# Kernel optimization log

Measured on AMD Instinct MI355X. Metric: run time of the kernel, lower is better.

Reference implementation:

```python
import jax, jax.numpy as jnp
import numpy as np

H = 1024


def setup_inputs() -> dict:
    key = jax.random.key(0)
    ks = jax.random.split(key, 8)
    B, S = 32, 2048
    query = jax.random.normal(ks[0], (B, 1, H), dtype=jnp.float32)
    keys = jax.random.normal(ks[1], (B, S, H), dtype=jnp.float32)
    s = 1.0 / np.sqrt(H)
    Wa_w = jax.random.uniform(ks[2], (H, H), jnp.float32, -s, s)
    Wa_b = jax.random.uniform(ks[3], (H,), jnp.float32, -s, s)
    Ua_w = jax.random.uniform(ks[4], (H, H), jnp.float32, -s, s)
    Ua_b = jax.random.uniform(ks[5], (H,), jnp.float32, -s, s)
    Va_w = jax.random.uniform(ks[6], (1, H), jnp.float32, -s, s)
    Va_b = jax.random.uniform(ks[7], (1,), jnp.float32, -s, s)
    return {"query": query, "keys": keys, "Wa_w": Wa_w, "Wa_b": Wa_b,
            "Ua_w": Ua_w, "Ua_b": Ua_b, "Va_w": Va_w, "Va_b": Va_b}


def reference(query, keys, Wa_w, Wa_b, Ua_w, Ua_b, Va_w, Va_b):
    # query: [B,1,H]; keys: [B,S,H]
    q_proj = jnp.einsum('boh,kh->bok', query, Wa_w) + Wa_b      # [B,1,H], broadcasts over S
    k_proj = jnp.einsum('bsh,kh->bsk', keys, Ua_w) + Ua_b       # [B,S,H]
    e = jnp.tanh(q_proj + k_proj)                               # [B,S,H]
    scores = jnp.einsum('bsh,h->bs', e, Va_w[0]) + Va_b[0]      # [B,S]
    weights = jax.nn.softmax(scores, axis=1)[:, None, :]        # [B,1,S]
    context = jnp.einsum('bos,bsh->boh', weights, keys)         # [B,1,H]
    return (context, weights)
```

## Files before the change

### kernel.cpp

```cpp
#include <hip/hip_runtime.h>
#include <hip/hip_bf16.h>

#define H 1024
#define B 32
#define S 2048

typedef __attribute__((ext_vector_type(8))) short bf16x8;
typedef __attribute__((ext_vector_type(4))) float f32x4;

union U4 { uint4 u; bf16x8 b; };

__device__ __forceinline__ unsigned short f2bf(float f) {
    unsigned u = __float_as_uint(f);
    unsigned r = (u + 0x7fffu + ((u >> 16) & 1u)) >> 16;
    return (unsigned short)r;
}

__device__ __forceinline__ uint4 pack8(float4 x, float4 y) {
    uint4 p;
    p.x = (unsigned)f2bf(x.x) | ((unsigned)f2bf(x.y) << 16);
    p.y = (unsigned)f2bf(x.z) | ((unsigned)f2bf(x.w) << 16);
    p.z = (unsigned)f2bf(y.x) | ((unsigned)f2bf(y.y) << 16);
    p.w = (unsigned)f2bf(y.z) | ((unsigned)f2bf(y.w) << 16);
    return p;
}

__device__ __forceinline__ float ftanh(float x) {
    float x2 = __builtin_amdgcn_fmed3f(x + x, -30.f, 30.f);
    float e = __expf(x2);
    return 1.f - 2.f * __builtin_amdgcn_rcpf(e + 1.f);
}

__device__ __forceinline__ void async_copy16(const void* g, void* l) {
    __builtin_amdgcn_global_load_lds(
        (const __attribute__((address_space(1))) unsigned int*)g,
        (__attribute__((address_space(3))) unsigned int*)l, 16, 0, 0);
}

__global__ void k0_swizzle(const float* __restrict__ Ua, uint4* __restrict__ UaSw) {
    int t = blockIdx.x * 256 + threadIdx.x;
    int lane = t & 63;
    int nt = (t >> 6) & 7;
    int kc = (t >> 9) & 31;
    int nb = t >> 14;
    int n = nb * 128 + nt * 16 + (lane & 15);
    int k = kc * 32 + ((lane >> 4) & 3) * 8;
    const float4* src = (const float4*)(Ua + (size_t)n * H + k);
    UaSw[t] = pack8(src[0], src[1]);
}

__global__ __launch_bounds__(256) void k1_qproj(
    const float* __restrict__ q, const float* __restrict__ Wa,
    const float* __restrict__ Wab, const float* __restrict__ Uab,
    float* __restrict__ qp) {
    int b = blockIdx.y;
    int t = threadIdx.x;
    int n = blockIdx.x * 64 + (t >> 2);
    int quarter = t & 3;
    __shared__ float qs[H];
    for (int i = t; i < H; i += 256) qs[i] = q[b * H + i];
    __syncthreads();
    const float4* wr = (const float4*)(Wa + (size_t)n * H + quarter * 256);
    const float* qq = qs + quarter * 256;
    float acc = 0.f;
#pragma unroll 4
    for (int i = 0; i < 64; i++) {
        float4 w = wr[i];
        acc += qq[i * 4 + 0] * w.x + qq[i * 4 + 1] * w.y +
               qq[i * 4 + 2] * w.z + qq[i * 4 + 3] * w.w;
    }
    acc += __shfl_xor(acc, 1, 64);
    acc += __shfl_xor(acc, 2, 64);
    if (quarter == 0) qp[b * H + n] = acc + Wab[n] + Uab[n];
}

__global__ __launch_bounds__(256, 3) void k2_scores(
    const float* __restrict__ keys, const uint4* __restrict__ UaSw,
    const float* __restrict__ qp, const float* __restrict__ Vaw,
    float* __restrict__ sp) {
    __shared__ uint4 As[2][512];
    __shared__ uint4 Bs[2][512];
    __shared__ float part[2][128];

    const int tid = threadIdx.x;
    const int lane = tid & 63;
    const int wave = tid >> 6;
    const int wm = wave >> 1, wn = wave & 1;
    const int lid = blockIdx.x;
    const int c = lid & 7;
    const int qq = lid >> 3;
    const int nb = qq & 7;
    const int mb = (qq >> 3) * 8 + c;
    const int b = mb >> 4;
    const int s0 = (mb & 15) << 7;

    const int el = tid & 63;
    const int srow0 = s0 + (tid >> 6) * 16 + (el & 15);
    const int srow1 = srow0 + 64;
    const int kofs = ((el >> 4) & 3) * 8;
    const float4* ka0 = (const float4*)(keys + ((size_t)b * S + srow0) * H + kofs);
    const float4* ka1 = (const float4*)(keys + ((size_t)b * S + srow1) * H + kofs);
    const uint4* srcB = UaSw + (size_t)nb * 32 * 512;

    f32x4 acc[4][4];
#pragma unroll
    for (int mt = 0; mt < 4; mt++)
#pragma unroll
        for (int nt = 0; nt < 4; nt++) acc[mt][nt] = (f32x4){0.f, 0.f, 0.f, 0.f};

    float4 x0 = ka0[0], y0 = ka0[1], x1 = ka1[0], y1 = ka1[1];
    async_copy16(srcB + tid,       &Bs[0][tid]);
    async_copy16(srcB + tid + 256, &Bs[0][tid + 256]);
    As[0][tid]       = pack8(x0, y0);
    As[0][tid + 256] = pack8(x1, y1);
    x0 = ka0[8]; y0 = ka0[9]; x1 = ka1[8]; y1 = ka1[9];
    __syncthreads();

    for (int kc = 0; kc < 32; kc++) {
        const int cur = kc & 1, nxt = cur ^ 1;
        if (kc < 31) {
            async_copy16(srcB + (size_t)(kc + 1) * 512 + tid,       &Bs[nxt][tid]);
            async_copy16(srcB + (size_t)(kc + 1) * 512 + tid + 256, &Bs[nxt][tid + 256]);
            As[nxt][tid]       = pack8(x0, y0);
            As[nxt][tid + 256] = pack8(x1, y1);
            if (kc < 30) {
                x0 = ka0[(kc + 2) * 8]; y0 = ka0[(kc + 2) * 8 + 1];
                x1 = ka1[(kc + 2) * 8]; y1 = ka1[(kc + 2) * 8 + 1];
            }
        }
        U4 af[4], bf[4];
#pragma unroll
        for (int mt = 0; mt < 4; mt++) af[mt].u = As[cur][(wm * 4 + mt) * 64 + lane];
#pragma unroll
        for (int nt = 0; nt < 4; nt++) bf[nt].u = Bs[cur][(wn * 4 + nt) * 64 + lane];
#pragma unroll
        for (int mt = 0; mt < 4; mt++)
#pragma unroll
            for (int nt = 0; nt < 4; nt++)
                acc[mt][nt] = __builtin_amdgcn_mfma_f32_16x16x32_bf16(
                    af[mt].b, bf[nt].b, acc[mt][nt], 0, 0, 0);
        __syncthreads();
    }

    const int col = lane & 15, qd = lane >> 4;
    float qv[4], vv[4];
#pragma unroll
    for (int nt = 0; nt < 4; nt++) {
        int n = nb * 128 + (wn * 4 + nt) * 16 + col;
        qv[nt] = qp[b * H + n];
        vv[nt] = Vaw[n];
    }
#pragma unroll
    for (int mt = 0; mt < 4; mt++) {
        float rs[4] = {0.f, 0.f, 0.f, 0.f};
#pragma unroll
        for (int nt = 0; nt < 4; nt++)
#pragma unroll
            for (int r = 0; r < 4; r++)
                rs[r] += ftanh(acc[mt][nt][r] + qv[nt]) * vv[nt];
#pragma unroll
        for (int r = 0; r < 4; r++) {
            float v = rs[r];
            v += __shfl_xor(v, 1, 64);
            v += __shfl_xor(v, 2, 64);
            v += __shfl_xor(v, 4, 64);
            v += __shfl_xor(v, 8, 64);
            if (col == 0) part[wn][wm * 64 + mt * 16 + qd * 4 + r] = v;
        }
    }
    __syncthreads();
    if (tid < 128)
        sp[(size_t)nb * B * S + b * S + s0 + tid] = part[0][tid] + part[1][tid];
}

__global__ __launch_bounds__(256) void k4_ctx(const float* __restrict__ keys,
                                              const float* __restrict__ sp,
                                              float* __restrict__ out) {
    int sc = blockIdx.x, b = blockIdx.y;
    int t = threadIdx.x;
    __shared__ float red[256];
    __shared__ float wl[64];

    float v[8];
#pragma unroll
    for (int i = 0; i < 8; i++) {
        int s = i * 256 + t;
        float sum = 0.f;
#pragma unroll
        for (int nb = 0; nb < 8; nb++) sum += sp[(size_t)nb * B * S + b * S + s];
        v[i] = sum;
    }
    float lm = -1e30f;
#pragma unroll
    for (int i = 0; i < 8; i++) lm = fmaxf(lm, v[i]);
    red[t] = lm;
    __syncthreads();
    for (int s = 128; s > 0; s >>= 1) {
        if (t < s) red[t] = fmaxf(red[t], red[t + s]);
        __syncthreads();
    }
    float m = red[0];
    __syncthreads();
    float ls = 0.f;
#pragma unroll
    for (int i = 0; i < 8; i++) ls += __expf(v[i] - m);
    red[t] = ls;
    __syncthreads();
    for (int s = 128; s > 0; s >>= 1) {
        if (t < s) red[t] += red[t + s];
        __syncthreads();
    }
    float inv = 1.f / red[0];

    if (t < 64) {
        int s = sc * 64 + t;
        float sum = 0.f;
#pragma unroll
        for (int nb = 0; nb < 8; nb++) sum += sp[(size_t)nb * B * S + b * S + s];
        float w = __expf(sum - m) * inv;
        wl[t] = w;
        out[B * H + b * S + s] = w;
    }
    __syncthreads();

    const float4* kp = (const float4*)(keys + ((size_t)b * S + sc * 64) * H) + t;
    float4 acc = {0.f, 0.f, 0.f, 0.f};
#pragma unroll 8
    for (int s = 0; s < 64; s++) {
        float4 kv = kp[(size_t)s * 256];
        float w = wl[s];
        acc.x += w * kv.x; acc.y += w * kv.y;
        acc.z += w * kv.z; acc.w += w * kv.w;
    }
    float* dst = out + b * H + t * 4;
    atomicAdd(dst + 0, acc.x);
    atomicAdd(dst + 1, acc.y);
    atomicAdd(dst + 2, acc.z);
    atomicAdd(dst + 3, acc.w);
}

extern "C" void kernel_launch(void* const* d_in, const int* in_sizes, int n_in,
                              void* d_out, int out_size, void* d_ws, size_t ws_size,
                              hipStream_t stream) {
    const float* query = (const float*)d_in[0];
    const float* keys  = (const float*)d_in[1];
    const float* Wa_w  = (const float*)d_in[2];
    const float* Wa_b  = (const float*)d_in[3];
    const float* Ua_w  = (const float*)d_in[4];
    const float* Ua_b  = (const float*)d_in[5];
    const float* Va_w  = (const float*)d_in[6];
    float* out = (float*)d_out;

    uint4* UaSw = (uint4*)d_ws;
    float* qp = (float*)((char*)d_ws + (2u << 20));
    float* sp = (float*)((char*)d_ws + (2u << 20) + (128u << 10));

    hipMemsetAsync(d_out, 0, B * H * sizeof(float), stream);

    k0_swizzle<<<512, 256, 0, stream>>>(Ua_w, UaSw);
    k1_qproj<<<dim3(16, B), 256, 0, stream>>>(query, Wa_w, Wa_b, Ua_b, qp);
    k2_scores<<<4096, 256, 0, stream>>>(keys, UaSw, qp, Va_w, sp);
    k4_ctx<<<dim3(32, B), 256, 0, stream>>>(keys, sp, out);
}
```

Measured before the change: 650.0 us.

## Pre-convert keys to bf16 fragment layout and feed score GEMM and context from it

Adds a pass that converts keys once into a bf16 buffer already laid out as MFMA fragments. The score GEMM then loads A and B fragments straight into registers with register double-buffering, with no LDS and no per-block fp32-to-bf16 packing. The context kernel now reads the bf16 keys, drops the atomics and the memset, and each block computes the full softmax. This aims to halve the repeated fp32 key traffic across the 8 column blocks, at the cost of an extra 128MB workspace write, a workspace-size-gated fallback, and bf16 precision in the context sum.

After: 592.1 us. 1.1x faster.

```diff
diff --git a/kernel.cpp b/kernel.cpp
--- a/kernel.cpp
+++ b/kernel.cpp
@@ -49,6 +49,19 @@
     UaSw[t] = pack8(src[0], src[1]);
 }
 
+__global__ __launch_bounds__(256) void ka_swz(const float* __restrict__ keys,
+                                              uint4* __restrict__ Abf) {
+    size_t g = (size_t)blockIdx.x * 256 + threadIdx.x;
+    int lane = (int)(g & 63);
+    size_t u = g >> 6;
+    int kc = (int)(u & 31);
+    size_t stile = u >> 5;
+    size_t row = stile * 16 + (lane & 15);
+    int col = kc * 32 + ((lane >> 4) & 3) * 8;
+    const float4* src = (const float4*)(keys + row * H + col);
+    Abf[g] = pack8(src[0], src[1]);
+}
+
 __global__ __launch_bounds__(256) void k1_qproj(
     const float* __restrict__ q, const float* __restrict__ Wa,
     const float* __restrict__ Wab, const float* __restrict__ Uab,
@@ -74,14 +87,172 @@
     if (quarter == 0) qp[b * H + n] = acc + Wab[n] + Uab[n];
 }
 
-__global__ __launch_bounds__(256, 3) void k2_scores(
+__global__ __launch_bounds__(256, 2) void k2_scores2(
+    const uint4* __restrict__ Abf, const uint4* __restrict__ UaSw,
+    const float* __restrict__ qp, const float* __restrict__ Vaw,
+    float* __restrict__ sp) {
+    const int tid = threadIdx.x;
+    const int lane = tid & 63;
+    const int wm = tid >> 6;
+    const int lid = blockIdx.x;
+    const int c = lid & 7;
+    const int qq = lid >> 3;
+    const int nb = qq & 7;
+    const int mb = (qq >> 3) * 8 + c;
+    const int b = mb >> 4;
+    const int s0 = (mb & 15) << 7;
+
+    const int stile0 = mb * 8 + wm * 2;
+    const uint4* pa = Abf + (size_t)stile0 * 2048 + lane;
+    const uint4* pb = UaSw + (size_t)nb * 16384 + lane;
+
+    f32x4 acc[2][8];
+#pragma unroll
+    for (int mt = 0; mt < 2; mt++)
+#pragma unroll
+        for (int nt = 0; nt < 8; nt++) acc[mt][nt] = (f32x4){0.f, 0.f, 0.f, 0.f};
+
+    U4 ca[2], cb[8], na[2], nbf[8];
+    ca[0].u = pa[0];
+    ca[1].u = pa[2048];
+#pragma unroll
+    for (int nt = 0; nt < 8; nt++) cb[nt].u = pb[nt * 64];
+
+    for (int kc = 0; kc < 32; kc++) {
+        if (kc < 31) {
+            na[0].u = pa[(kc + 1) * 64];
+            na[1].u = pa[(kc + 1) * 64 + 2048];
+#pragma unroll
+            for (int nt = 0; nt < 8; nt++) nbf[nt].u = pb[(kc + 1) * 512 + nt * 64];
+        }
+#pragma unroll
+        for (int nt = 0; nt < 8; nt++)
+#pragma unroll
+            for (int mt = 0; mt < 2; mt++)
+                acc[mt][nt] = __builtin_amdgcn_mfma_f32_16x16x32_bf16(
+                    ca[mt].b, cb[nt].b, acc[mt][nt], 0, 0, 0);
+        if (kc < 31) {
+            ca[0] = na[0]; ca[1] = na[1];
+#pragma unroll
+            for (int nt = 0; nt < 8; nt++) cb[nt] = nbf[nt];
+        }
+    }
+
+    const int col = lane & 15, qd = lane >> 4;
+    float qv[8], vv[8];
+#pragma unroll
+    for (int nt = 0; nt < 8; nt++) {
+        int n = nb * 128 + nt * 16 + col;
+        qv[nt] = qp[b * H + n];
+        vv[nt] = Vaw[n];
+    }
+#pragma unroll
+    for (int mt = 0; mt < 2; mt++) {
+        float rs[4] = {0.f, 0.f, 0.f, 0.f};
+#pragma unroll
+        for (int nt = 0; nt < 8; nt++)
+#pragma unroll
+            for (int r = 0; r < 4; r++)
+                rs[r] += ftanh(acc[mt][nt][r] + qv[nt]) * vv[nt];
+#pragma unroll
+        for (int r = 0; r < 4; r++) {
+            float v = rs[r];
+            v += __shfl_xor(v, 1, 64);
+            v += __shfl_xor(v, 2, 64);
+            v += __shfl_xor(v, 4, 64);
+            v += __shfl_xor(v, 8, 64);
+            if (col == 0)
+                sp[(size_t)nb * B * S + b * S + s0 + wm * 32 + mt * 16 + qd * 4 + r] = v;
+        }
+    }
+}
+
+__global__ __launch_bounds__(256) void k4_ctx2(const uint4* __restrict__ Abf,
+                                               const float* __restrict__ sp,
+                                               float* __restrict__ out) {
+    int kcg = blockIdx.x, b = blockIdx.y;
+    int t = threadIdx.x;
+    __shared__ float red[256];
+    __shared__ float wl[S];
+
+    float v[8];
+#pragma unroll
+    for (int i = 0; i < 8; i++) {
+        int s = i * 256 + t;
+        float sum = 0.f;
+#pragma unroll
+        for (int nb = 0; nb < 8; nb++) sum += sp[(size_t)nb * B * S + b * S + s];
+        v[i] = sum;
+    }
+    float lm = -1e30f;
+#pragma unroll
+    for (int i = 0; i < 8; i++) lm = fmaxf(lm, v[i]);
+    red[t] = lm;
+    __syncthreads();
+    for (int s = 128; s > 0; s >>= 1) {
+        if (t < s) red[t] = fmaxf(red[t], red[t + s]);
+        __syncthreads();
+    }
+    float m = red[0];
+    __syncthreads();
+    float ls = 0.f;
+#pragma unroll
+    for (int i = 0; i < 8; i++) ls += __expf(v[i] - m);
+    red[t] = ls;
+    __syncthreads();
+    for (int s = 128; s > 0; s >>= 1) {
+        if (t < s) red[t] += red[t + s];
+        __syncthreads();
+    }
+    float inv = 1.f / red[0];
+#pragma unroll
+    for (int i = 0; i < 8; i++) {
+        int s = i * 256 + t;
+        float w = __expf(v[i] - m) * inv;
+        wl[s] = w;
+        if (kcg == 0) out[B * H + b * S + s] = w;
+    }
+    __syncthreads();
+
+    const int wv = t >> 6, lane = t & 63, qd = lane >> 4, colr = lane & 15;
+    const int kc = kcg * 4 + wv;
+    float a8[8] = {0.f, 0.f, 0.f, 0.f, 0.f, 0.f, 0.f, 0.f};
+    const uint4* base = Abf + ((size_t)(b * 128) * 32 + kc) * 64 + lane;
+    for (int st = 0; st < 128; st++) {
+        uint4 f = base[(size_t)st * 2048];
+        float w = wl[st * 16 + colr];
+        a8[0] += w * __uint_as_float(f.x << 16);
+        a8[1] += w * __uint_as_float(f.x & 0xffff0000u);
+        a8[2] += w * __uint_as_float(f.y << 16);
+        a8[3] += w * __uint_as_float(f.y & 0xffff0000u);
+        a8[4] += w * __uint_as_float(f.z << 16);
+        a8[5] += w * __uint_as_float(f.z & 0xffff0000u);
+        a8[6] += w * __uint_as_float(f.w << 16);
+        a8[7] += w * __uint_as_float(f.w & 0xffff0000u);
+    }
+#pragma unroll
+    for (int j = 0; j < 8; j++) {
+        float vj = a8[j];
+        vj += __shfl_xor(vj, 1, 64);
+        vj += __shfl_xor(vj, 2, 64);
+        vj += __shfl_xor(vj, 4, 64);
+        vj += __shfl_xor(vj, 8, 64);
+        a8[j] = vj;
+    }
+    if (colr == 0) {
+        int colbase = kc * 32 + qd * 8;
+#pragma unroll
+        for (int j = 0; j < 8; j++) out[b * H + colbase + j] = a8[j];
+    }
+}
+
+__global__ __launch_bounds__(256, 3) void k2_scores_fb(
     const float* __restrict__ keys, const uint4* __restrict__ UaSw,
     const float* __restrict__ qp, const float* __restrict__ Vaw,
     float* __restrict__ sp) {
     __shared__ uint4 As[2][512];
     __shared__ uint4 Bs[2][512];
     __shared__ float part[2][128];
-
     const int tid = threadIdx.x;
     const int lane = tid & 63;
     const int wave = tid >> 6;
@@ -93,7 +264,6 @@
     const int mb = (qq >> 3) * 8 + c;
     const int b = mb >> 4;
     const int s0 = (mb & 15) << 7;
-
     const int el = tid & 63;
     const int srow0 = s0 + (tid >> 6) * 16 + (el & 15);
     const int srow1 = srow0 + 64;
@@ -101,13 +271,11 @@
     const float4* ka0 = (const float4*)(keys + ((size_t)b * S + srow0) * H + kofs);
     const float4* ka1 = (const float4*)(keys + ((size_t)b * S + srow1) * H + kofs);
     const uint4* srcB = UaSw + (size_t)nb * 32 * 512;
-
     f32x4 acc[4][4];
 #pragma unroll
     for (int mt = 0; mt < 4; mt++)
 #pragma unroll
         for (int nt = 0; nt < 4; nt++) acc[mt][nt] = (f32x4){0.f, 0.f, 0.f, 0.f};
-
     float4 x0 = ka0[0], y0 = ka0[1], x1 = ka1[0], y1 = ka1[1];
     async_copy16(srcB + tid,       &Bs[0][tid]);
     async_copy16(srcB + tid + 256, &Bs[0][tid + 256]);
@@ -115,7 +283,6 @@
     As[0][tid + 256] = pack8(x1, y1);
     x0 = ka0[8]; y0 = ka0[9]; x1 = ka1[8]; y1 = ka1[9];
     __syncthreads();
-
     for (int kc = 0; kc < 32; kc++) {
         const int cur = kc & 1, nxt = cur ^ 1;
         if (kc < 31) {
@@ -141,7 +308,6 @@
                     af[mt].b, bf[nt].b, acc[mt][nt], 0, 0, 0);
         __syncthreads();
     }
-
     const int col = lane & 15, qd = lane >> 4;
     float qv[4], vv[4];
 #pragma unroll
@@ -173,14 +339,13 @@
         sp[(size_t)nb * B * S + b * S + s0 + tid] = part[0][tid] + part[1][tid];
 }
 
-__global__ __launch_bounds__(256) void k4_ctx(const float* __restrict__ keys,
-                                              const float* __restrict__ sp,
-                                              float* __restrict__ out) {
+__global__ __launch_bounds__(256) void k4_ctx_fb(const float* __restrict__ keys,
+                                                 const float* __restrict__ sp,
+                                                 float* __restrict__ out) {
     int sc = blockIdx.x, b = blockIdx.y;
     int t = threadIdx.x;
     __shared__ float red[256];
     __shared__ float wl[64];
-
     float v[8];
 #pragma unroll
     for (int i = 0; i < 8; i++) {
@@ -211,7 +376,6 @@
         __syncthreads();
     }
     float inv = 1.f / red[0];
-
     if (t < 64) {
         int s = sc * 64 + t;
         float sum = 0.f;
@@ -222,7 +386,6 @@
         out[B * H + b * S + s] = w;
     }
     __syncthreads();
-
     const float4* kp = (const float4*)(keys + ((size_t)b * S + sc * 64) * H) + t;
     float4 acc = {0.f, 0.f, 0.f, 0.f};
 #pragma unroll 8
@@ -254,11 +417,20 @@
     uint4* UaSw = (uint4*)d_ws;
     float* qp = (float*)((char*)d_ws + (2u << 20));
     float* sp = (float*)((char*)d_ws + (2u << 20) + (128u << 10));
-
-    hipMemsetAsync(d_out, 0, B * H * sizeof(float), stream);
-
-    k0_swizzle<<<512, 256, 0, stream>>>(Ua_w, UaSw);
-    k1_qproj<<<dim3(16, B), 256, 0, stream>>>(query, Wa_w, Wa_b, Ua_b, qp);
-    k2_scores<<<4096, 256, 0, stream>>>(keys, UaSw, qp, Va_w, sp);
-    k4_ctx<<<dim3(32, B), 256, 0, stream>>>(keys, sp, out);
-}
+    uint4* Abf = (uint4*)((char*)d_ws + (8u << 20));
+    const size_t NEED = (size_t)(8u << 20) + ((size_t)128u << 20);
+
+    if (ws_size >= NEED) {
+        ka_swz<<<32768, 256, 0, stream>>>(keys, Abf);
+        k0_swizzle<<<512, 256, 0, stream>>>(Ua_w, UaSw);
+        k1_qproj<<<dim3(16, B), 256, 0, stream>>>(query, Wa_w, Wa_b, Ua_b, qp);
+        k2_scores2<<<4096, 256, 0, stream>>>(Abf, UaSw, qp, Va_w, sp);
+        k4_ctx2<<<dim3(8, B), 256, 0, stream>>>(Abf, sp, out);
+    } else {
+        hipMemsetAsync(d_out, 0, B * H * sizeof(float), stream);
+        k0_swizzle<<<512, 256, 0, stream>>>(Ua_w, UaSw);
+        k1_qproj<<<dim3(16, B), 256, 0, stream>>>(query, Wa_w, Wa_b, Ua_b, qp);
+        k2_scores_fb<<<4096, 256, 0, stream>>>(keys, UaSw, qp, Va_w, sp);
+        k4_ctx_fb<<<dim3(32, B), 256, 0, stream>>>(keys, sp, out);
+    }
+}
```

## Drop LDS staging in score GEMM, load fragments directly into registers

Applied to the files above, without the earlier changes.

The score GEMM kernel no longer stages keys and the pre-swizzled Ua weights through double-buffered shared memory. Each wave now owns a 64x128 tile and loads its A rows and B fragments straight from global memory into registers, with no block barriers. Tiles per block double (256 rows, 2048 blocks), occupancy drops to 2 blocks per SIMD, and keys are converted to bf16 with a cheaper pack (hardware cvt or round-half-up perm). The trade is more redundant global and L2 traffic for the B fragments, plus higher register pressure, in exchange for removing LDS writes and syncs.

New measurement: 703.3 us. +8.2%, slower.

```diff
diff --git a/kernel.cpp b/kernel.cpp
--- a/kernel.cpp
+++ b/kernel.cpp
@@ -16,7 +16,29 @@
     return (unsigned short)r;
 }
 
+__device__ __forceinline__ unsigned pk2(float a, float b) {
+#if __has_builtin(__builtin_amdgcn_cvt_pk_bf16_f32)
+    typedef __attribute__((ext_vector_type(2))) __bf16 bfp2;
+    union { bfp2 v; unsigned u; } p;
+    p.v = __builtin_amdgcn_cvt_pk_bf16_f32(a, b);
+    return p.u;
+#else
+    unsigned ua = __float_as_uint(a) + 0x8000u;
+    unsigned ub = __float_as_uint(b) + 0x8000u;
+    return __builtin_amdgcn_perm(ub, ua, 0x07060302u);
+#endif
+}
+
 __device__ __forceinline__ uint4 pack8(float4 x, float4 y) {
+    uint4 p;
+    p.x = pk2(x.x, x.y);
+    p.y = pk2(x.z, x.w);
+    p.z = pk2(y.x, y.y);
+    p.w = pk2(y.z, y.w);
+    return p;
+}
+
+__device__ __forceinline__ uint4 pack8_rne(float4 x, float4 y) {
     uint4 p;
     p.x = (unsigned)f2bf(x.x) | ((unsigned)f2bf(x.y) << 16);
     p.y = (unsigned)f2bf(x.z) | ((unsigned)f2bf(x.w) << 16);
@@ -29,12 +51,6 @@
     float x2 = __builtin_amdgcn_fmed3f(x + x, -30.f, 30.f);
     float e = __expf(x2);
     return 1.f - 2.f * __builtin_amdgcn_rcpf(e + 1.f);
-}
-
-__device__ __forceinline__ void async_copy16(const void* g, void* l) {
-    __builtin_amdgcn_global_load_lds(
-        (const __attribute__((address_space(1))) unsigned int*)g,
-        (__attribute__((address_space(3))) unsigned int*)l, 16, 0, 0);
 }
 
 __global__ void k0_swizzle(const float* __restrict__ Ua, uint4* __restrict__ UaSw) {
@@ -46,7 +62,7 @@
     int n = nb * 128 + nt * 16 + (lane & 15);
     int k = kc * 32 + ((lane >> 4) & 3) * 8;
     const float4* src = (const float4*)(Ua + (size_t)n * H + k);
-    UaSw[t] = pack8(src[0], src[1]);
+    UaSw[t] = pack8_rne(src[0], src[1]);
 }
 
 __global__ __launch_bounds__(256) void k1_qproj(
@@ -74,79 +90,67 @@
     if (quarter == 0) qp[b * H + n] = acc + Wab[n] + Uab[n];
 }
 
-__global__ __launch_bounds__(256, 3) void k2_scores(
+__global__ __launch_bounds__(256, 2) void k2_scores3(
     const float* __restrict__ keys, const uint4* __restrict__ UaSw,
     const float* __restrict__ qp, const float* __restrict__ Vaw,
     float* __restrict__ sp) {
-    __shared__ uint4 As[2][512];
-    __shared__ uint4 Bs[2][512];
-    __shared__ float part[2][128];
-
     const int tid = threadIdx.x;
     const int lane = tid & 63;
-    const int wave = tid >> 6;
-    const int wm = wave >> 1, wn = wave & 1;
+    const int wm = tid >> 6;
     const int lid = blockIdx.x;
     const int c = lid & 7;
-    const int qq = lid >> 3;
-    const int nb = qq & 7;
-    const int mb = (qq >> 3) * 8 + c;
-    const int b = mb >> 4;
-    const int s0 = (mb & 15) << 7;
-
-    const int el = tid & 63;
-    const int srow0 = s0 + (tid >> 6) * 16 + (el & 15);
-    const int srow1 = srow0 + 64;
-    const int kofs = ((el >> 4) & 3) * 8;
-    const float4* ka0 = (const float4*)(keys + ((size_t)b * S + srow0) * H + kofs);
-    const float4* ka1 = (const float4*)(keys + ((size_t)b * S + srow1) * H + kofs);
-    const uint4* srcB = UaSw + (size_t)nb * 32 * 512;
-
-    f32x4 acc[4][4];
+    const int qx = lid >> 3;
+    const int nb = qx & 7;
+    const int mblk = (qx >> 3) * 8 + c;
+    const int b = mblk >> 3;
+    const int s0 = (mblk & 7) << 8;
+
+    const int colq = (lane >> 4) & 3;
+    const float4* pa[4];
+#pragma unroll
+    for (int mt = 0; mt < 4; mt++) {
+        int row = s0 + wm * 64 + mt * 16 + (lane & 15);
+        pa[mt] = (const float4*)(keys + ((size_t)b * S + row) * H) + colq * 2;
+    }
+    const uint4* pb = UaSw + (size_t)nb * 16384 + lane;
+
+    f32x4 acc[4][8];
 #pragma unroll
     for (int mt = 0; mt < 4; mt++)
 #pragma unroll
-        for (int nt = 0; nt < 4; nt++) acc[mt][nt] = (f32x4){0.f, 0.f, 0.f, 0.f};
-
-    float4 x0 = ka0[0], y0 = ka0[1], x1 = ka1[0], y1 = ka1[1];
-    async_copy16(srcB + tid,       &Bs[0][tid]);
-    async_copy16(srcB + tid + 256, &Bs[0][tid + 256]);
-    As[0][tid]       = pack8(x0, y0);
-    As[0][tid + 256] = pack8(x1, y1);
-    x0 = ka0[8]; y0 = ka0[9]; x1 = ka1[8]; y1 = ka1[9];
-    __syncthreads();
+        for (int nt = 0; nt < 8; nt++) acc[mt][nt] = (f32x4){0.f, 0.f, 0.f, 0.f};
+
+    float4 xf[4], yf[4];
+#pragma unroll
+    for (int mt = 0; mt < 4; mt++) { xf[mt] = pa[mt][0]; yf[mt] = pa[mt][1]; }
 
     for (int kc = 0; kc < 32; kc++) {
-        const int cur = kc & 1, nxt = cur ^ 1;
+        U4 bfr[8];
+#pragma unroll
+        for (int nt = 0; nt < 8; nt++) bfr[nt].u = pb[kc * 512 + nt * 64];
+        U4 a[4];
+#pragma unroll
+        for (int mt = 0; mt < 4; mt++) a[mt].u = pack8(xf[mt], yf[mt]);
         if (kc < 31) {
-            async_copy16(srcB + (size_t)(kc + 1) * 512 + tid,       &Bs[nxt][tid]);
-            async_copy16(srcB + (size_t)(kc + 1) * 512 + tid + 256, &Bs[nxt][tid + 256]);
-            As[nxt][tid]       = pack8(x0, y0);
-            As[nxt][tid + 256] = pack8(x1, y1);
-            if (kc < 30) {
-                x0 = ka0[(kc + 2) * 8]; y0 = ka0[(kc + 2) * 8 + 1];
-                x1 = ka1[(kc + 2) * 8]; y1 = ka1[(kc + 2) * 8 + 1];
+#pragma unroll
+            for (int mt = 0; mt < 4; mt++) {
+                xf[mt] = pa[mt][(kc + 1) * 8];
+                yf[mt] = pa[mt][(kc + 1) * 8 + 1];
             }
         }
-        U4 af[4], bf[4];
-#pragma unroll
-        for (int mt = 0; mt < 4; mt++) af[mt].u = As[cur][(wm * 4 + mt) * 64 + lane];
-#pragma unroll
-        for (int nt = 0; nt < 4; nt++) bf[nt].u = Bs[cur][(wn * 4 + nt) * 64 + lane];
-#pragma unroll
-        for (int mt = 0; mt < 4; mt++)
-#pragma unroll
-            for (int nt = 0; nt < 4; nt++)
+#pragma unroll
+        for (int nt = 0; nt < 8; nt++)
+#pragma unroll
+            for (int mt = 0; mt < 4; mt++)
                 acc[mt][nt] = __builtin_amdgcn_mfma_f32_16x16x32_bf16(
-                    af[mt].b, bf[nt].b, acc[mt][nt], 0, 0, 0);
-        __syncthreads();
+                    a[mt].b, bfr[nt].b, acc[mt][nt], 0, 0, 0);
     }
 
     const int col = lane & 15, qd = lane >> 4;
-    float qv[4], vv[4];
-#pragma unroll
-    for (int nt = 0; nt < 4; nt++) {
-        int n = nb * 128 + (wn * 4 + nt) * 16 + col;
+    float qv[8], vv[8];
+#pragma unroll
+    for (int nt = 0; nt < 8; nt++) {
+        int n = nb * 128 + nt * 16 + col;
         qv[nt] = qp[b * H + n];
         vv[nt] = Vaw[n];
     }
@@ -154,7 +158,7 @@
     for (int mt = 0; mt < 4; mt++) {
         float rs[4] = {0.f, 0.f, 0.f, 0.f};
 #pragma unroll
-        for (int nt = 0; nt < 4; nt++)
+        for (int nt = 0; nt < 8; nt++)
 #pragma unroll
             for (int r = 0; r < 4; r++)
                 rs[r] += ftanh(acc[mt][nt][r] + qv[nt]) * vv[nt];
@@ -165,12 +169,13 @@
             v += __shfl_xor(v, 2, 64);
             v += __shfl_xor(v, 4, 64);
             v += __shfl_xor(v, 8, 64);
-            if (col == 0) part[wn][wm * 64 + mt * 16 + qd * 4 + r] = v;
+            rs[r] = v;
         }
-    }
-    __syncthreads();
-    if (tid < 128)
-        sp[(size_t)nb * B * S + b * S + s0 + tid] = part[0][tid] + part[1][tid];
+        if (col == 0) {
+            float4 st = {rs[0], rs[1], rs[2], rs[3]};
+            *(float4*)&sp[(size_t)nb * B * S + b * S + s0 + wm * 64 + mt * 16 + qd * 4] = st;
+        }
+    }
 }
 
 __global__ __launch_bounds__(256) void k4_ctx(const float* __restrict__ keys,
@@ -259,6 +264,6 @@
 
     k0_swizzle<<<512, 256, 0, stream>>>(Ua_w, UaSw);
     k1_qproj<<<dim3(16, B), 256, 0, stream>>>(query, Wa_w, Wa_b, Ua_b, qp);
-    k2_scores<<<4096, 256, 0, stream>>>(keys, UaSw, qp, Va_w, sp);
+    k2_scores3<<<2048, 256, 0, stream>>>(keys, UaSw, qp, Va_w, sp);
     k4_ctx<<<dim3(32, B), 256, 0, stream>>>(keys, sp, out);
 }
```
